# Kernel tuning notes

Hardware: AMD Instinct MI355X
Metric: run time of the kernel (lower is better)

## Reference

```python
import jax, jax.numpy as jnp
import numpy as np

TOP_K = 2


def setup_inputs() -> dict:
    key = jax.random.key(0)
    ks = jax.random.split(key, 5)
    B, N, C, FF, E = 2, 2048, 1024, 4096, 8
    x = jax.random.normal(ks[0], (B, N, C), dtype=jnp.float32)
    router_w = jax.random.normal(ks[1], (E, C), dtype=jnp.float32) * 0.02
    # xavier-uniform-like init for expert weights
    lim1 = np.sqrt(6.0 / (FF + C))
    expert_w1 = jax.random.uniform(ks[2], (E, FF, C), dtype=jnp.float32, minval=-lim1, maxval=lim1)
    expert_b1 = jnp.zeros((E, FF), dtype=jnp.float32)
    expert_w2 = jax.random.uniform(ks[3], (E, C, FF), dtype=jnp.float32, minval=-lim1, maxval=lim1)
    expert_b2 = jnp.zeros((E, C), dtype=jnp.float32)
    return {"x": x, "router_w": router_w, "expert_w1": expert_w1,
            "expert_b1": expert_b1, "expert_w2": expert_w2, "expert_b2": expert_b2}


def reference(x, router_w, expert_w1, expert_b1, expert_w2, expert_b2):
    # x: [B,N,C]; router_w: [E,C]; expert_w1: [E,FF,C]; expert_w2: [E,C,FF]
    router_logits = jnp.einsum('bnc,ec->bne', x, router_w)          # [B,N,E]
    router_probs = jax.nn.softmax(router_logits, axis=-1)
    expert_weights, expert_idx = jax.lax.top_k(router_probs, TOP_K)  # [B,N,K]
    expert_weights = expert_weights / (expert_weights.sum(axis=-1, keepdims=True) + 1e-9)
    # Dense all-expert FFN (avoids materializing per-token gathered weight matrices)
    h = jnp.einsum('bnc,efc->bnef', x, expert_w1) + expert_b1        # [B,N,E,FF]
    h = jax.nn.gelu(h, approximate=False)                            # torch nn.GELU = exact
    out_all = jnp.einsum('bnef,ecf->bnec', h, expert_w2) + expert_b2  # [B,N,E,C]
    # Gather top-k expert outputs and combine
    out_k = jnp.take_along_axis(out_all, expert_idx[..., None], axis=2)  # [B,N,K,C]
    return (out_k * expert_weights[..., None]).sum(axis=2)           # [B,N,C]
```

## Files before the change

### kernel.cpp

```cpp
#include <hip/hip_runtime.h>
#include <hip/hip_bf16.h>
#include <cstdint>

#define TTOK  4096
#define CDIM  1024
#define FFDIM 4096
#define NEXP  8


typedef short short8 __attribute__((ext_vector_type(8)));
typedef float f32x4 __attribute__((ext_vector_type(4)));

__device__ __forceinline__ unsigned short f2bf(float f) {
    unsigned int u = __float_as_uint(f);
    u = u + 0x7fffu + ((u >> 16) & 1u);
    return (unsigned short)(u >> 16);
}

__device__ __forceinline__ void gl_lds16(const unsigned short* g, unsigned short* l) {
    __builtin_amdgcn_global_load_lds(
        (const __attribute__((address_space(1))) unsigned int*)g,
        (__attribute__((address_space(3))) unsigned int*)l, 16, 0, 0);
}

__global__ void cast_kernel(const float* __restrict__ src, unsigned short* __restrict__ dst) {
    int i = blockIdx.x * blockDim.x + threadIdx.x;
    float4 v = reinterpret_cast<const float4*>(src)[i];
    ushort4 o;
    o.x = f2bf(v.x); o.y = f2bf(v.y); o.z = f2bf(v.z); o.w = f2bf(v.w);
    reinterpret_cast<ushort4*>(dst)[i] = o;
}

__global__ void router_kernel(const float* __restrict__ x, const float* __restrict__ rw,
                              int* __restrict__ counts, int* __restrict__ btok,
                              float* __restrict__ bgate) {
    const int wave = threadIdx.x >> 6;
    const int lane = threadIdx.x & 63;
    const int t = blockIdx.x * 4 + wave;
    const float* xr = x + (size_t)t * CDIM;

    float acc[NEXP];
#pragma unroll
    for (int e = 0; e < NEXP; e++) acc[e] = 0.f;
    for (int c = lane; c < CDIM; c += 64) {
        float xv = xr[c];
#pragma unroll
        for (int e = 0; e < NEXP; e++) acc[e] += xv * rw[e * CDIM + c];
    }
#pragma unroll
    for (int e = 0; e < NEXP; e++) {
#pragma unroll
        for (int off = 32; off > 0; off >>= 1) acc[e] += __shfl_down(acc[e], off, 64);
    }
    if (lane == 0) {
        float mx = acc[0];
#pragma unroll
        for (int e = 1; e < NEXP; e++) mx = fmaxf(mx, acc[e]);
        float p[NEXP]; float s = 0.f;
#pragma unroll
        for (int e = 0; e < NEXP; e++) { p[e] = expf(acc[e] - mx); s += p[e]; }
        int i0 = 0;
#pragma unroll
        for (int e = 1; e < NEXP; e++) if (p[e] > p[i0]) i0 = e;
        int i1 = (i0 == 0) ? 1 : 0;
#pragma unroll
        for (int e = 0; e < NEXP; e++) if (e != i0 && p[e] > p[i1]) i1 = e;
        float pr0 = p[i0] / s, pr1 = p[i1] / s;
        float rs = 1.f / (pr0 + pr1 + 1e-9f);
        float w0 = pr0 * rs, w1 = pr1 * rs;
        int pos = atomicAdd(&counts[i0], 1);
        btok[i0 * TTOK + pos] = t; bgate[i0 * TTOK + pos] = w0;
        pos = atomicAdd(&counts[i1], 1);
        btok[i1 * TTOK + pos] = t; bgate[i1 * TTOK + pos] = w1;
    }
}

__global__ void offsets_kernel(const int* __restrict__ counts, int* __restrict__ offsets) {
    if (threadIdx.x == 0 && blockIdx.x == 0) {
        int s = 0;
        for (int e = 0; e < NEXP; e++) { offsets[e] = s; s += counts[e]; }
        offsets[NEXP] = s;
    }
}


__global__ __launch_bounds__(256) void gemm1f_kernel(
    const unsigned short* __restrict__ xb, const unsigned short* __restrict__ w1b,
    const float* __restrict__ b1, const int* __restrict__ counts,
    const int* __restrict__ offsets, const int* __restrict__ btok,
    unsigned short* __restrict__ H) {
    const int e = blockIdx.z;
    const int cnt = counts[e];
    const int m0 = blockIdx.y * 128;
    if (m0 >= cnt) return;
    const int n0 = blockIdx.x * 128;
    const int po = offsets[e];

    __shared__ uint4 smem4[2048];
    unsigned short* smem = (unsigned short*)smem4;

    const int tid = threadIdx.x;
    const int wave = tid >> 6, lane = tid & 63;
    const int wm = (wave >> 1) << 6, wn = (wave & 1) << 6;
    const int lm = lane & 15, kq = lane >> 4;

    const int sr = tid >> 2;
    const int sc = (tid & 3) << 3;
    const int tA0 = btok[e * TTOK + min(m0 + sr, cnt - 1)];
    const int tA1 = btok[e * TTOK + min(m0 + 64 + sr, cnt - 1)];
    const unsigned short* ga0 = xb + (size_t)tA0 * CDIM + sc;
    const unsigned short* ga1 = xb + (size_t)tA1 * CDIM + sc;
    const unsigned short* gb0 = w1b + ((size_t)e * FFDIM + n0 + sr) * CDIM + sc;
    const unsigned short* gb1 = gb0 + (size_t)64 * CDIM;

    f32x4 acc[4][4];
#pragma unroll
    for (int i = 0; i < 4; i++)
#pragma unroll
        for (int j = 0; j < 4; j++) { f32x4 z = {0.f, 0.f, 0.f, 0.f}; acc[i][j] = z; }

    {
        unsigned short* base = smem;
        gl_lds16(ga0, base + tid * 8);
        gl_lds16(ga1, base + 64 * 32 + tid * 8);
        gl_lds16(gb0, base + 4096 + tid * 8);
        gl_lds16(gb1, base + 4096 + 64 * 32 + tid * 8);
    }

    for (int k0 = 0; k0 < CDIM; k0 += 32) {
        const int cur = (k0 >> 5) & 1;
        __syncthreads();
        if (k0 + 32 < CDIM) {
            unsigned short* base = smem + (cur ^ 1) * 8192;
            gl_lds16(ga0 + k0 + 32, base + tid * 8);
            gl_lds16(ga1 + k0 + 32, base + 64 * 32 + tid * 8);
            gl_lds16(gb0 + k0 + 32, base + 4096 + tid * 8);
            gl_lds16(gb1 + k0 + 32, base + 4096 + 64 * 32 + tid * 8);
        }
        const unsigned short* As = smem + cur * 8192;
        const unsigned short* Bs = As + 4096;
        short8 af[4], bfr[4];
#pragma unroll
        for (int i = 0; i < 4; i++) af[i] = *reinterpret_cast<const short8*>(&As[(wm + i * 16 + lm) * 32 + kq * 8]);
#pragma unroll
        for (int j = 0; j < 4; j++) bfr[j] = *reinterpret_cast<const short8*>(&Bs[(wn + j * 16 + lm) * 32 + kq * 8]);
#pragma unroll
        for (int i = 0; i < 4; i++)
#pragma unroll
            for (int j = 0; j < 4; j++)
                acc[i][j] = __builtin_amdgcn_mfma_f32_16x16x32_bf16(af[i], bfr[j], acc[i][j], 0, 0, 0);
    }
    __syncthreads();

    float bias[4];
#pragma unroll
    for (int j = 0; j < 4; j++) bias[j] = b1[e * FFDIM + n0 + wn + j * 16 + lm];

    unsigned short* Cs = smem;
#pragma unroll
    for (int p = 0; p < 2; p++) {
        if ((wave >> 1) == p) {
#pragma unroll
            for (int i = 0; i < 4; i++) {
#pragma unroll
                for (int r = 0; r < 4; r++) {
                    const int row = i * 16 + kq * 4 + r;
#pragma unroll
                    for (int j = 0; j < 4; j++) {
                        float h = acc[i][j][r] + bias[j];
                        float g = 0.5f * h * (1.f + erff(h * 0.70710678118654752f));
                        Cs[row * 128 + wn + j * 16 + lm] = f2bf(g);
                    }
                }
            }
        }
        __syncthreads();
#pragma unroll
        for (int q = 0; q < 4; q++) {
            const int c = q * 256 + tid;
            const int row = c >> 4;
            const int col8 = (c & 15) << 3;
            const int mrow = m0 + p * 64 + row;
            if (mrow < cnt)
                *reinterpret_cast<uint4*>(&H[(size_t)(po + mrow) * FFDIM + n0 + col8]) =
                    *reinterpret_cast<const uint4*>(&Cs[row * 128 + col8]);
        }
        __syncthreads();
    }
}

__global__ __launch_bounds__(256) void gemm2f_kernel(
    const unsigned short* __restrict__ H, const unsigned short* __restrict__ w2b,
    const float* __restrict__ b2, const int* __restrict__ counts,
    const int* __restrict__ offsets, const int* __restrict__ btok,
    const float* __restrict__ bgate, float* __restrict__ out) {
    const int e = blockIdx.z;
    const int cnt = counts[e];
    const int m0 = (blockIdx.y >> 1) * 128;
    const int ks = blockIdx.y & 1;
    if (m0 >= cnt) return;
    const int n0 = blockIdx.x * 128;
    const int po = offsets[e];

    __shared__ uint4 smem4[2048];
    unsigned short* smem = (unsigned short*)smem4;

    const int tid = threadIdx.x;
    const int wave = tid >> 6, lane = tid & 63;
    const int wm = (wave >> 1) << 6, wn = (wave & 1) << 6;
    const int lm = lane & 15, kq = lane >> 4;

    const int sr = tid >> 2;
    const int sc = (tid & 3) << 3;
    const int r0 = min(m0 + sr, cnt - 1);
    const int r1 = min(m0 + 64 + sr, cnt - 1);
    const unsigned short* ga0 = H + (size_t)(po + r0) * FFDIM + ks * 2048 + sc;
    const unsigned short* ga1 = H + (size_t)(po + r1) * FFDIM + ks * 2048 + sc;
    const unsigned short* gb0 = w2b + ((size_t)e * CDIM + n0 + sr) * FFDIM + ks * 2048 + sc;
    const unsigned short* gb1 = gb0 + (size_t)64 * FFDIM;

    f32x4 acc[4][4];
#pragma unroll
    for (int i = 0; i < 4; i++)
#pragma unroll
        for (int j = 0; j < 4; j++) { f32x4 z = {0.f, 0.f, 0.f, 0.f}; acc[i][j] = z; }

    {
        unsigned short* base = smem;
        gl_lds16(ga0, base + tid * 8);
        gl_lds16(ga1, base + 64 * 32 + tid * 8);
        gl_lds16(gb0, base + 4096 + tid * 8);
        gl_lds16(gb1, base + 4096 + 64 * 32 + tid * 8);
    }

    for (int k0 = 0; k0 < 2048; k0 += 32) {
        const int cur = (k0 >> 5) & 1;
        __syncthreads();
        if (k0 + 32 < 2048) {
            unsigned short* base = smem + (cur ^ 1) * 8192;
            gl_lds16(ga0 + k0 + 32, base + tid * 8);
            gl_lds16(ga1 + k0 + 32, base + 64 * 32 + tid * 8);
            gl_lds16(gb0 + k0 + 32, base + 4096 + tid * 8);
            gl_lds16(gb1 + k0 + 32, base + 4096 + 64 * 32 + tid * 8);
        }
        const unsigned short* As = smem + cur * 8192;
        const unsigned short* Bs = As + 4096;
        short8 af[4], bfr[4];
#pragma unroll
        for (int i = 0; i < 4; i++) af[i] = *reinterpret_cast<const short8*>(&As[(wm + i * 16 + lm) * 32 + kq * 8]);
#pragma unroll
        for (int j = 0; j < 4; j++) bfr[j] = *reinterpret_cast<const short8*>(&Bs[(wn + j * 16 + lm) * 32 + kq * 8]);
#pragma unroll
        for (int i = 0; i < 4; i++)
#pragma unroll
            for (int j = 0; j < 4; j++)
                acc[i][j] = __builtin_amdgcn_mfma_f32_16x16x32_bf16(af[i], bfr[j], acc[i][j], 0, 0, 0);
    }

    float bias[4];
#pragma unroll
    for (int j = 0; j < 4; j++) bias[j] = (ks == 0) ? b2[e * CDIM + n0 + wn + j * 16 + lm] : 0.f;

#pragma unroll
    for (int i = 0; i < 4; i++) {
#pragma unroll
        for (int r = 0; r < 4; r++) {
            const int mrow = m0 + wm + i * 16 + kq * 4 + r;
            if (mrow < cnt) {
                const int tok = btok[e * TTOK + mrow];
                const float g = bgate[e * TTOK + mrow];
                float* orow = out + (size_t)tok * CDIM;
#pragma unroll
                for (int j = 0; j < 4; j++)
                    atomicAdd(orow + n0 + wn + j * 16 + lm, g * (acc[i][j][r] + bias[j]));
            }
        }
    }
}


__global__ __launch_bounds__(256) void gemm1_kernel(
    const unsigned short* __restrict__ xb, const float* __restrict__ w1,
    const float* __restrict__ b1, const int* __restrict__ counts,
    const int* __restrict__ offsets, const int* __restrict__ btok,
    unsigned short* __restrict__ H) {
    const int e = blockIdx.z;
    const int cnt = counts[e];
    const int m0 = blockIdx.y * 128;
    if (m0 >= cnt) return;
    const int n0 = blockIdx.x * 128;
    const int po = offsets[e];

    __shared__ unsigned short As[128][32];
    __shared__ unsigned short Bs[128][32];

    const int tid = threadIdx.x;
    const int wave = tid >> 6, lane = tid & 63;
    const int wm = (wave >> 1) << 6, wn = (wave & 1) << 6;
    const int lm = lane & 15, kq = lane >> 4;

    f32x4 acc[4][4];
#pragma unroll
    for (int i = 0; i < 4; i++)
#pragma unroll
        for (int j = 0; j < 4; j++) { f32x4 z = {0.f, 0.f, 0.f, 0.f}; acc[i][j] = z; }

    const float* w1e = w1 + (size_t)e * FFDIM * CDIM;
    const int arow = tid >> 1;
    const int acolb = (tid & 1) * 16;
    int tokA = -1;
    if (m0 + arow < cnt) tokA = btok[e * TTOK + m0 + arow];
    const int brow = tid >> 1;
    const int bcol = (tid & 1) * 16;

    for (int k0 = 0; k0 < CDIM; k0 += 32) {
        uint4 a0 = {0, 0, 0, 0}, a1 = {0, 0, 0, 0};
        if (tokA >= 0) {
            const uint4* src = reinterpret_cast<const uint4*>(xb + (size_t)tokA * CDIM + k0 + acolb);
            a0 = src[0]; a1 = src[1];
        }
        *reinterpret_cast<uint4*>(&As[arow][acolb]) = a0;
        *reinterpret_cast<uint4*>(&As[arow][acolb + 8]) = a1;
        {
            const float* src = w1e + (size_t)(n0 + brow) * CDIM + k0 + bcol;
            ushort4* dst = reinterpret_cast<ushort4*>(&Bs[brow][bcol]);
#pragma unroll
            for (int q = 0; q < 4; q++) {
                float4 v = reinterpret_cast<const float4*>(src)[q];
                ushort4 o; o.x = f2bf(v.x); o.y = f2bf(v.y); o.z = f2bf(v.z); o.w = f2bf(v.w);
                dst[q] = o;
            }
        }
        __syncthreads();
        short8 af[4], bfr[4];
#pragma unroll
        for (int i = 0; i < 4; i++) af[i] = *reinterpret_cast<const short8*>(&As[wm + i * 16 + lm][kq * 8]);
#pragma unroll
        for (int j = 0; j < 4; j++) bfr[j] = *reinterpret_cast<const short8*>(&Bs[wn + j * 16 + lm][kq * 8]);
#pragma unroll
        for (int i = 0; i < 4; i++)
#pragma unroll
            for (int j = 0; j < 4; j++)
                acc[i][j] = __builtin_amdgcn_mfma_f32_16x16x32_bf16(af[i], bfr[j], acc[i][j], 0, 0, 0);
        __syncthreads();
    }

#pragma unroll
    for (int j = 0; j < 4; j++) {
        const int fcol = n0 + wn + j * 16 + lm;
        const float bias = b1[e * FFDIM + fcol];
#pragma unroll
        for (int i = 0; i < 4; i++) {
#pragma unroll
            for (int r = 0; r < 4; r++) {
                const int mrow = m0 + wm + i * 16 + kq * 4 + r;
                if (mrow < cnt) {
                    float h = acc[i][j][r] + bias;
                    float g = 0.5f * h * (1.f + erff(h * 0.70710678118654752f));
                    H[(size_t)(po + mrow) * FFDIM + fcol] = f2bf(g);
                }
            }
        }
    }
}

__global__ __launch_bounds__(256) void gemm2_kernel(
    const unsigned short* __restrict__ H, const float* __restrict__ w2,
    const float* __restrict__ b2, const int* __restrict__ counts,
    const int* __restrict__ offsets, const int* __restrict__ btok,
    const float* __restrict__ bgate, float* __restrict__ out) {
    const int e = blockIdx.z;
    const int cnt = counts[e];
    const int m0 = blockIdx.y * 128;
    if (m0 >= cnt) return;
    const int n0 = blockIdx.x * 128;
    const int po = offsets[e];

    __shared__ unsigned short As[128][32];
    __shared__ unsigned short Bs[128][32];

    const int tid = threadIdx.x;
    const int wave = tid >> 6, lane = tid & 63;
    const int wm = (wave >> 1) << 6, wn = (wave & 1) << 6;
    const int lm = lane & 15, kq = lane >> 4;

    f32x4 acc[4][4];
#pragma unroll
    for (int i = 0; i < 4; i++)
#pragma unroll
        for (int j = 0; j < 4; j++) { f32x4 z = {0.f, 0.f, 0.f, 0.f}; acc[i][j] = z; }

    const float* w2e = w2 + (size_t)e * CDIM * FFDIM;
    const int arow = tid >> 1;
    const int acolb = (tid & 1) * 16;
    const bool aval = (m0 + arow < cnt);
    const unsigned short* asrc = H + (size_t)(po + m0 + arow) * FFDIM + acolb;
    const int brow = tid >> 1;
    const int bcol = (tid & 1) * 16;

    for (int k0 = 0; k0 < FFDIM; k0 += 32) {
        uint4 a0 = {0, 0, 0, 0}, a1 = {0, 0, 0, 0};
        if (aval) {
            const uint4* src = reinterpret_cast<const uint4*>(asrc + k0);
            a0 = src[0]; a1 = src[1];
        }
        *reinterpret_cast<uint4*>(&As[arow][acolb]) = a0;
        *reinterpret_cast<uint4*>(&As[arow][acolb + 8]) = a1;
        {
            const float* src = w2e + (size_t)(n0 + brow) * FFDIM + k0 + bcol;
            ushort4* dst = reinterpret_cast<ushort4*>(&Bs[brow][bcol]);
#pragma unroll
            for (int q = 0; q < 4; q++) {
                float4 v = reinterpret_cast<const float4*>(src)[q];
                ushort4 o; o.x = f2bf(v.x); o.y = f2bf(v.y); o.z = f2bf(v.z); o.w = f2bf(v.w);
                dst[q] = o;
            }
        }
        __syncthreads();
        short8 af[4], bfr[4];
#pragma unroll
        for (int i = 0; i < 4; i++) af[i] = *reinterpret_cast<const short8*>(&As[wm + i * 16 + lm][kq * 8]);
#pragma unroll
        for (int j = 0; j < 4; j++) bfr[j] = *reinterpret_cast<const short8*>(&Bs[wn + j * 16 + lm][kq * 8]);
#pragma unroll
        for (int i = 0; i < 4; i++)
#pragma unroll
            for (int j = 0; j < 4; j++)
                acc[i][j] = __builtin_amdgcn_mfma_f32_16x16x32_bf16(af[i], bfr[j], acc[i][j], 0, 0, 0);
        __syncthreads();
    }

    float bias[4];
#pragma unroll
    for (int j = 0; j < 4; j++) bias[j] = b2[e * CDIM + n0 + wn + j * 16 + lm];

#pragma unroll
    for (int i = 0; i < 4; i++) {
#pragma unroll
        for (int r = 0; r < 4; r++) {
            const int mrow = m0 + wm + i * 16 + kq * 4 + r;
            if (mrow < cnt) {
                const int tok = btok[e * TTOK + mrow];
                const float g = bgate[e * TTOK + mrow];
                float* orow = out + (size_t)tok * CDIM;
#pragma unroll
                for (int j = 0; j < 4; j++) {
                    const int c = n0 + wn + j * 16 + lm;
                    atomicAdd(orow + c, g * (acc[i][j][r] + bias[j]));
                }
            }
        }
    }
}

extern "C" void kernel_launch(void* const* d_in, const int* in_sizes, int n_in,
                              void* d_out, int out_size, void* d_ws, size_t ws_size,
                              hipStream_t stream) {
    const float* x  = (const float*)d_in[0];
    const float* rw = (const float*)d_in[1];
    const float* w1 = (const float*)d_in[2];
    const float* b1 = (const float*)d_in[3];
    const float* w2 = (const float*)d_in[4];
    const float* b2 = (const float*)d_in[5];
    float* out = (float*)d_out;

    char* ws = (char*)d_ws;
    int*   counts  = (int*)ws;
    int*   offsets = (int*)(ws + 64);
    int*   btok    = (int*)(ws + 4096);
    float* bgate   = (float*)(ws + 4096 + 131072);

    hipMemsetAsync(d_out, 0, (size_t)out_size * sizeof(float), stream);
    hipMemsetAsync(counts, 0, 64, stream);

    const bool fast = ws_size >= ((size_t)137 << 20);

    if (fast) {
        unsigned short* xb = (unsigned short*)(ws + ((size_t)1 << 20));
        unsigned short* Wb = (unsigned short*)(ws + ((size_t)9 << 20));
        unsigned short* H  = (unsigned short*)(ws + ((size_t)73 << 20));

        cast_kernel<<<(TTOK * CDIM) / (256 * 4), 256, 0, stream>>>(x, xb);
        router_kernel<<<TTOK / 4, 256, 0, stream>>>(x, rw, counts, btok, bgate);
        offsets_kernel<<<1, 64, 0, stream>>>(counts, offsets);
        cast_kernel<<<(NEXP * FFDIM * CDIM) / (256 * 4), 256, 0, stream>>>(w1, Wb);
        gemm1f_kernel<<<dim3(FFDIM / 128, TTOK / 128, NEXP), 256, 0, stream>>>(
            xb, Wb, b1, counts, offsets, btok, H);
        cast_kernel<<<(NEXP * CDIM * FFDIM) / (256 * 4), 256, 0, stream>>>(w2, Wb);
        gemm2f_kernel<<<dim3(CDIM / 128, (TTOK / 128) * 2, NEXP), 256, 0, stream>>>(
            H, Wb, b2, counts, offsets, btok, bgate, out);
    } else {
        unsigned short* xb = (unsigned short*)(ws + ((size_t)1 << 20));
        unsigned short* H  = (unsigned short*)(ws + ((size_t)16 << 20));

        cast_kernel<<<(TTOK * CDIM) / (256 * 4), 256, 0, stream>>>(x, xb);
        router_kernel<<<TTOK / 4, 256, 0, stream>>>(x, rw, counts, btok, bgate);
        offsets_kernel<<<1, 64, 0, stream>>>(counts, offsets);
        gemm1_kernel<<<dim3(FFDIM / 128, TTOK / 128, NEXP), 256, 0, stream>>>(
            xb, w1, b1, counts, offsets, btok, H);
        gemm2_kernel<<<dim3(CDIM / 128, TTOK / 128, NEXP), 256, 0, stream>>>(
            H, w2, b2, counts, offsets, btok, bgate, out);
    }
}
```

Before: 718.0 us.

## Rework expert GEMMs into 256x256 tiles with 4-stage swizzled LDS pipeline

```diff
diff --git a/kernel.cpp b/kernel.cpp
--- a/kernel.cpp
+++ b/kernel.cpp
@@ -22,6 +22,16 @@
         (const __attribute__((address_space(1))) unsigned int*)g,
         (__attribute__((address_space(3))) unsigned int*)l, 16, 0, 0);
 }
+
+__device__ __forceinline__ int swz_off(int row, int kq) {
+    const int line = row >> 1;
+    const int cp = ((((row & 1) << 2) | kq) ^ (line & 7));
+    return line * 64 + cp * 8;
+}
+
+#define SBAR() do { __builtin_amdgcn_sched_barrier(0); \
+                    __builtin_amdgcn_s_barrier();      \
+                    __builtin_amdgcn_sched_barrier(0); } while (0)
 
 __global__ void cast_kernel(const float* __restrict__ src, unsigned short* __restrict__ dst) {
     int i = blockIdx.x * blockDim.x + threadIdx.x;
@@ -84,195 +94,268 @@
 }
 
 
-__global__ __launch_bounds__(256) void gemm1f_kernel(
+__global__ __launch_bounds__(512, 2) void gemm1p_kernel(
     const unsigned short* __restrict__ xb, const unsigned short* __restrict__ w1b,
     const float* __restrict__ b1, const int* __restrict__ counts,
     const int* __restrict__ offsets, const int* __restrict__ btok,
     unsigned short* __restrict__ H) {
     const int e = blockIdx.z;
     const int cnt = counts[e];
-    const int m0 = blockIdx.y * 128;
+    const int m0 = blockIdx.y * 256;
     if (m0 >= cnt) return;
-    const int n0 = blockIdx.x * 128;
+    const int n0 = blockIdx.x * 256;
     const int po = offsets[e];
-
-    __shared__ uint4 smem4[2048];
-    unsigned short* smem = (unsigned short*)smem4;
+    const int NT = CDIM / 32;
+
+    __shared__ uint4 smem4[8192];
+    unsigned short* S = (unsigned short*)smem4;
 
     const int tid = threadIdx.x;
-    const int wave = tid >> 6, lane = tid & 63;
-    const int wm = (wave >> 1) << 6, wn = (wave & 1) << 6;
+    const int wid = tid >> 6, lane = tid & 63;
     const int lm = lane & 15, kq = lane >> 4;
-
-    const int sr = tid >> 2;
-    const int sc = (tid & 3) << 3;
-    const int tA0 = btok[e * TTOK + min(m0 + sr, cnt - 1)];
-    const int tA1 = btok[e * TTOK + min(m0 + 64 + sr, cnt - 1)];
-    const unsigned short* ga0 = xb + (size_t)tA0 * CDIM + sc;
-    const unsigned short* ga1 = xb + (size_t)tA1 * CDIM + sc;
-    const unsigned short* gb0 = w1b + ((size_t)e * FFDIM + n0 + sr) * CDIM + sc;
-    const unsigned short* gb1 = gb0 + (size_t)64 * CDIM;
-
-    f32x4 acc[4][4];
-#pragma unroll
-    for (int i = 0; i < 4; i++)
-#pragma unroll
-        for (int j = 0; j < 4; j++) { f32x4 z = {0.f, 0.f, 0.f, 0.f}; acc[i][j] = z; }
-
-    {
-        unsigned short* base = smem;
-        gl_lds16(ga0, base + tid * 8);
-        gl_lds16(ga1, base + 64 * 32 + tid * 8);
-        gl_lds16(gb0, base + 4096 + tid * 8);
-        gl_lds16(gb1, base + 4096 + 64 * 32 + tid * 8);
-    }
-
-    for (int k0 = 0; k0 < CDIM; k0 += 32) {
-        const int cur = (k0 >> 5) & 1;
-        __syncthreads();
-        if (k0 + 32 < CDIM) {
-            unsigned short* base = smem + (cur ^ 1) * 8192;
-            gl_lds16(ga0 + k0 + 32, base + tid * 8);
-            gl_lds16(ga1 + k0 + 32, base + 64 * 32 + tid * 8);
-            gl_lds16(gb0 + k0 + 32, base + 4096 + tid * 8);
-            gl_lds16(gb1 + k0 + 32, base + 4096 + 64 * 32 + tid * 8);
-        }
-        const unsigned short* As = smem + cur * 8192;
-        const unsigned short* Bs = As + 4096;
-        short8 af[4], bfr[4];
-#pragma unroll
-        for (int i = 0; i < 4; i++) af[i] = *reinterpret_cast<const short8*>(&As[(wm + i * 16 + lm) * 32 + kq * 8]);
-#pragma unroll
-        for (int j = 0; j < 4; j++) bfr[j] = *reinterpret_cast<const short8*>(&Bs[(wn + j * 16 + lm) * 32 + kq * 8]);
-#pragma unroll
-        for (int i = 0; i < 4; i++)
-#pragma unroll
-            for (int j = 0; j < 4; j++)
-                acc[i][j] = __builtin_amdgcn_mfma_f32_16x16x32_bf16(af[i], bfr[j], acc[i][j], 0, 0, 0);
-    }
+    const int wr = wid >> 2, wc = wid & 3;
+
+    const int sline = tid >> 3;
+    const int c128s = (tid & 7) ^ (sline & 7);
+    const int prty  = c128s >> 2;
+    const int skc   = (c128s & 3) << 3;
+    const int ar0 = min(m0 + (sline << 1) + prty, cnt - 1);
+    const int ar1 = min(m0 + 128 + (sline << 1) + prty, cnt - 1);
+    const unsigned short* asrc0 = xb + (size_t)btok[e * TTOK + ar0] * CDIM + skc;
+    const unsigned short* asrc1 = xb + (size_t)btok[e * TTOK + ar1] * CDIM + skc;
+    const unsigned short* bsrc0 = w1b + ((size_t)e * FFDIM + n0 + (sline << 1) + prty) * CDIM + skc;
+    const unsigned short* bsrc1 = bsrc0 + (size_t)128 * CDIM;
+
+    int offA[8], offB[4];
+#pragma unroll
+    for (int f = 0; f < 8; f++) offA[f] = swz_off(wr * 128 + f * 16 + lm, kq);
+#pragma unroll
+    for (int g = 0; g < 4; g++) offB[g] = swz_off(wc * 64 + g * 16 + lm, kq);
+
+    f32x4 acc[8][4];
+#pragma unroll
+    for (int f = 0; f < 8; f++)
+#pragma unroll
+        for (int g = 0; g < 4; g++) { f32x4 z = {0.f, 0.f, 0.f, 0.f}; acc[f][g] = z; }
+
+#pragma unroll
+    for (int tt = 0; tt < 3; tt++) {
+        unsigned short* Sa = S + tt * 16384;
+        unsigned short* Sb = Sa + 8192;
+        const int ko = tt * 32;
+        gl_lds16(asrc0 + ko, Sa + tid * 8);
+        gl_lds16(bsrc0 + ko, Sb + tid * 8);
+        gl_lds16(asrc1 + ko, Sa + (512 + tid) * 8);
+        gl_lds16(bsrc1 + ko, Sb + (512 + tid) * 8);
+    }
+    asm volatile("s_waitcnt vmcnt(8)" ::: "memory");
+    SBAR();
+
+    for (int t = 0; t < NT; ++t) {
+        unsigned short* Ab = S + (t & 3) * 16384;
+        unsigned short* Bb = Ab + 8192;
+        int ts = t + 3; if (ts >= NT) ts -= NT;
+        unsigned short* Sa = S + (ts & 3) * 16384;
+        unsigned short* Sb = Sa + 8192;
+        const int ko = ts * 32;
+
+        short8 bf[4];
+        {
+            short8 af[4];
+#pragma unroll
+            for (int f = 0; f < 4; f++) af[f] = *reinterpret_cast<const short8*>(&Ab[offA[f]]);
+#pragma unroll
+            for (int g = 0; g < 4; g++) bf[g] = *reinterpret_cast<const short8*>(&Bb[offB[g]]);
+            gl_lds16(asrc0 + ko, Sa + tid * 8);
+            gl_lds16(bsrc0 + ko, Sb + tid * 8);
+            SBAR();
+            __builtin_amdgcn_s_setprio(1);
+#pragma unroll
+            for (int f = 0; f < 4; f++)
+#pragma unroll
+                for (int g = 0; g < 4; g++)
+                    acc[f][g] = __builtin_amdgcn_mfma_f32_16x16x32_bf16(af[f], bf[g], acc[f][g], 0, 0, 0);
+            __builtin_amdgcn_s_setprio(0);
+            SBAR();
+        }
+        {
+            short8 af[4];
+#pragma unroll
+            for (int f = 0; f < 4; f++) af[f] = *reinterpret_cast<const short8*>(&Ab[offA[4 + f]]);
+            gl_lds16(asrc1 + ko, Sa + (512 + tid) * 8);
+            gl_lds16(bsrc1 + ko, Sb + (512 + tid) * 8);
+            asm volatile("s_waitcnt vmcnt(8)" ::: "memory");
+            SBAR();
+            __builtin_amdgcn_s_setprio(1);
+#pragma unroll
+            for (int f = 0; f < 4; f++)
+#pragma unroll
+                for (int g = 0; g < 4; g++)
+                    acc[4 + f][g] = __builtin_amdgcn_mfma_f32_16x16x32_bf16(af[f], bf[g], acc[4 + f][g], 0, 0, 0);
+            __builtin_amdgcn_s_setprio(0);
+            SBAR();
+        }
+    }
+
+    asm volatile("s_waitcnt vmcnt(0)" ::: "memory");
     __syncthreads();
 
     float bias[4];
 #pragma unroll
-    for (int j = 0; j < 4; j++) bias[j] = b1[e * FFDIM + n0 + wn + j * 16 + lm];
-
-    unsigned short* Cs = smem;
-#pragma unroll
-    for (int p = 0; p < 2; p++) {
-        if ((wave >> 1) == p) {
-#pragma unroll
-            for (int i = 0; i < 4; i++) {
-#pragma unroll
-                for (int r = 0; r < 4; r++) {
-                    const int row = i * 16 + kq * 4 + r;
-#pragma unroll
-                    for (int j = 0; j < 4; j++) {
-                        float h = acc[i][j][r] + bias[j];
-                        float g = 0.5f * h * (1.f + erff(h * 0.70710678118654752f));
-                        Cs[row * 128 + wn + j * 16 + lm] = f2bf(g);
-                    }
-                }
+    for (int g = 0; g < 4; g++) bias[g] = b1[e * FFDIM + n0 + wc * 64 + g * 16 + lm];
+
+    unsigned short* Cs = S;
+#pragma unroll
+    for (int f = 0; f < 8; f++) {
+#pragma unroll
+        for (int r = 0; r < 4; r++) {
+            const int row = wr * 128 + f * 16 + kq * 4 + r;
+#pragma unroll
+            for (int g = 0; g < 4; g++) {
+                const int col = wc * 64 + g * 16 + lm;
+                float h = acc[f][g][r] + bias[g];
+                float gl = 0.5f * h * (1.f + erff(h * 0.70710678118654752f));
+                Cs[(row * 256 + col) ^ ((row & 7) << 3)] = f2bf(gl);
             }
         }
-        __syncthreads();
-#pragma unroll
-        for (int q = 0; q < 4; q++) {
-            const int c = q * 256 + tid;
-            const int row = c >> 4;
-            const int col8 = (c & 15) << 3;
-            const int mrow = m0 + p * 64 + row;
-            if (mrow < cnt)
-                *reinterpret_cast<uint4*>(&H[(size_t)(po + mrow) * FFDIM + n0 + col8]) =
-                    *reinterpret_cast<const uint4*>(&Cs[row * 128 + col8]);
-        }
-        __syncthreads();
-    }
-}
-
-__global__ __launch_bounds__(256) void gemm2f_kernel(
+    }
+    __syncthreads();
+#pragma unroll
+    for (int q = 0; q < 16; q++) {
+        const int cq = q * 512 + tid;
+        const int row = cq >> 5;
+        const int cc = cq & 31;
+        const int mrow = m0 + row;
+        if (mrow < cnt)
+            *reinterpret_cast<uint4*>(&H[(size_t)(po + mrow) * FFDIM + n0 + cc * 8]) =
+                *reinterpret_cast<const uint4*>(&Cs[(row * 256 + cc * 8) ^ ((row & 7) << 3)]);
+    }
+}
+
+__global__ __launch_bounds__(512, 2) void gemm2p_kernel(
     const unsigned short* __restrict__ H, const unsigned short* __restrict__ w2b,
     const float* __restrict__ b2, const int* __restrict__ counts,
     const int* __restrict__ offsets, const int* __restrict__ btok,
     const float* __restrict__ bgate, float* __restrict__ out) {
     const int e = blockIdx.z;
     const int cnt = counts[e];
-    const int m0 = (blockIdx.y >> 1) * 128;
+    const int m0 = (blockIdx.y >> 1) * 256;
     const int ks = blockIdx.y & 1;
     if (m0 >= cnt) return;
-    const int n0 = blockIdx.x * 128;
+    const int n0 = blockIdx.x * 256;
     const int po = offsets[e];
-
-    __shared__ uint4 smem4[2048];
-    unsigned short* smem = (unsigned short*)smem4;
+    const int NT = 2048 / 32;
+
+    __shared__ uint4 smem4[8192];
+    unsigned short* S = (unsigned short*)smem4;
 
     const int tid = threadIdx.x;
-    const int wave = tid >> 6, lane = tid & 63;
-    const int wm = (wave >> 1) << 6, wn = (wave & 1) << 6;
+    const int wid = tid >> 6, lane = tid & 63;
     const int lm = lane & 15, kq = lane >> 4;
-
-    const int sr = tid >> 2;
-    const int sc = (tid & 3) << 3;
-    const int r0 = min(m0 + sr, cnt - 1);
-    const int r1 = min(m0 + 64 + sr, cnt - 1);
-    const unsigned short* ga0 = H + (size_t)(po + r0) * FFDIM + ks * 2048 + sc;
-    const unsigned short* ga1 = H + (size_t)(po + r1) * FFDIM + ks * 2048 + sc;
-    const unsigned short* gb0 = w2b + ((size_t)e * CDIM + n0 + sr) * FFDIM + ks * 2048 + sc;
-    const unsigned short* gb1 = gb0 + (size_t)64 * FFDIM;
-
-    f32x4 acc[4][4];
-#pragma unroll
-    for (int i = 0; i < 4; i++)
-#pragma unroll
-        for (int j = 0; j < 4; j++) { f32x4 z = {0.f, 0.f, 0.f, 0.f}; acc[i][j] = z; }
-
-    {
-        unsigned short* base = smem;
-        gl_lds16(ga0, base + tid * 8);
-        gl_lds16(ga1, base + 64 * 32 + tid * 8);
-        gl_lds16(gb0, base + 4096 + tid * 8);
-        gl_lds16(gb1, base + 4096 + 64 * 32 + tid * 8);
-    }
-
-    for (int k0 = 0; k0 < 2048; k0 += 32) {
-        const int cur = (k0 >> 5) & 1;
-        __syncthreads();
-        if (k0 + 32 < 2048) {
-            unsigned short* base = smem + (cur ^ 1) * 8192;
-            gl_lds16(ga0 + k0 + 32, base + tid * 8);
-            gl_lds16(ga1 + k0 + 32, base + 64 * 32 + tid * 8);
-            gl_lds16(gb0 + k0 + 32, base + 4096 + tid * 8);
-            gl_lds16(gb1 + k0 + 32, base + 4096 + 64 * 32 + tid * 8);
-        }
-        const unsigned short* As = smem + cur * 8192;
-        const unsigned short* Bs = As + 4096;
-        short8 af[4], bfr[4];
-#pragma unroll
-        for (int i = 0; i < 4; i++) af[i] = *reinterpret_cast<const short8*>(&As[(wm + i * 16 + lm) * 32 + kq * 8]);
-#pragma unroll
-        for (int j = 0; j < 4; j++) bfr[j] = *reinterpret_cast<const short8*>(&Bs[(wn + j * 16 + lm) * 32 + kq * 8]);
-#pragma unroll
-        for (int i = 0; i < 4; i++)
-#pragma unroll
-            for (int j = 0; j < 4; j++)
-                acc[i][j] = __builtin_amdgcn_mfma_f32_16x16x32_bf16(af[i], bfr[j], acc[i][j], 0, 0, 0);
-    }
+    const int wr = wid >> 2, wc = wid & 3;
+
+    const int sline = tid >> 3;
+    const int c128s = (tid & 7) ^ (sline & 7);
+    const int prty  = c128s >> 2;
+    const int skc   = (c128s & 3) << 3;
+    const int koff  = ks * 2048;
+    const int ar0 = min(m0 + (sline << 1) + prty, cnt - 1);
+    const int ar1 = min(m0 + 128 + (sline << 1) + prty, cnt - 1);
+    const unsigned short* asrc0 = H + (size_t)(po + ar0) * FFDIM + koff + skc;
+    const unsigned short* asrc1 = H + (size_t)(po + ar1) * FFDIM + koff + skc;
+    const unsigned short* bsrc0 = w2b + ((size_t)e * CDIM + n0 + (sline << 1) + prty) * FFDIM + koff + skc;
+    const unsigned short* bsrc1 = bsrc0 + (size_t)128 * FFDIM;
+
+    int offA[8], offB[4];
+#pragma unroll
+    for (int f = 0; f < 8; f++) offA[f] = swz_off(wr * 128 + f * 16 + lm, kq);
+#pragma unroll
+    for (int g = 0; g < 4; g++) offB[g] = swz_off(wc * 64 + g * 16 + lm, kq);
+
+    f32x4 acc[8][4];
+#pragma unroll
+    for (int f = 0; f < 8; f++)
+#pragma unroll
+        for (int g = 0; g < 4; g++) { f32x4 z = {0.f, 0.f, 0.f, 0.f}; acc[f][g] = z; }
+
+#pragma unroll
+    for (int tt = 0; tt < 3; tt++) {
+        unsigned short* Sa = S + tt * 16384;
+        unsigned short* Sb = Sa + 8192;
+        const int ko = tt * 32;
+        gl_lds16(asrc0 + ko, Sa + tid * 8);
+        gl_lds16(bsrc0 + ko, Sb + tid * 8);
+        gl_lds16(asrc1 + ko, Sa + (512 + tid) * 8);
+        gl_lds16(bsrc1 + ko, Sb + (512 + tid) * 8);
+    }
+    asm volatile("s_waitcnt vmcnt(8)" ::: "memory");
+    SBAR();
+
+    for (int t = 0; t < NT; ++t) {
+        unsigned short* Ab = S + (t & 3) * 16384;
+        unsigned short* Bb = Ab + 8192;
+        int ts = t + 3; if (ts >= NT) ts -= NT;
+        unsigned short* Sa = S + (ts & 3) * 16384;
+        unsigned short* Sb = Sa + 8192;
+        const int ko = ts * 32;
+
+        short8 bf[4];
+        {
+            short8 af[4];
+#pragma unroll
+            for (int f = 0; f < 4; f++) af[f] = *reinterpret_cast<const short8*>(&Ab[offA[f]]);
+#pragma unroll
+            for (int g = 0; g < 4; g++) bf[g] = *reinterpret_cast<const short8*>(&Bb[offB[g]]);
+            gl_lds16(asrc0 + ko, Sa + tid * 8);
+            gl_lds16(bsrc0 + ko, Sb + tid * 8);
+            SBAR();
+            __builtin_amdgcn_s_setprio(1);
+#pragma unroll
+            for (int f = 0; f < 4; f++)
+#pragma unroll
+                for (int g = 0; g < 4; g++)
+                    acc[f][g] = __builtin_amdgcn_mfma_f32_16x16x32_bf16(af[f], bf[g], acc[f][g], 0, 0, 0);
+            __builtin_amdgcn_s_setprio(0);
+            SBAR();
+        }
+        {
+            short8 af[4];
+#pragma unroll
+            for (int f = 0; f < 4; f++) af[f] = *reinterpret_cast<const short8*>(&Ab[offA[4 + f]]);
+            gl_lds16(asrc1 + ko, Sa + (512 + tid) * 8);
+            gl_lds16(bsrc1 + ko, Sb + (512 + tid) * 8);
+            asm volatile("s_waitcnt vmcnt(8)" ::: "memory");
+            SBAR();
+            __builtin_amdgcn_s_setprio(1);
+#pragma unroll
+            for (int f = 0; f < 4; f++)
+#pragma unroll
+                for (int g = 0; g < 4; g++)
+                    acc[4 + f][g] = __builtin_amdgcn_mfma_f32_16x16x32_bf16(af[f], bf[g], acc[4 + f][g], 0, 0, 0);
+            __builtin_amdgcn_s_setprio(0);
+            SBAR();
+        }
+    }
+
+    asm volatile("s_waitcnt vmcnt(0)" ::: "memory");
 
     float bias[4];
 #pragma unroll
-    for (int j = 0; j < 4; j++) bias[j] = (ks == 0) ? b2[e * CDIM + n0 + wn + j * 16 + lm] : 0.f;
-
-#pragma unroll
-    for (int i = 0; i < 4; i++) {
+    for (int g = 0; g < 4; g++)
+        bias[g] = (ks == 0) ? b2[e * CDIM + n0 + wc * 64 + g * 16 + lm] : 0.f;
+
+#pragma unroll
+    for (int f = 0; f < 8; f++) {
 #pragma unroll
         for (int r = 0; r < 4; r++) {
-            const int mrow = m0 + wm + i * 16 + kq * 4 + r;
+            const int mrow = m0 + wr * 128 + f * 16 + kq * 4 + r;
             if (mrow < cnt) {
                 const int tok = btok[e * TTOK + mrow];
-                const float g = bgate[e * TTOK + mrow];
-                float* orow = out + (size_t)tok * CDIM;
-#pragma unroll
-                for (int j = 0; j < 4; j++)
-                    atomicAdd(orow + n0 + wn + j * 16 + lm, g * (acc[i][j][r] + bias[j]));
+                const float g8 = bgate[e * TTOK + mrow];
+                float* orow = out + (size_t)tok * CDIM + n0;
+#pragma unroll
+                for (int g = 0; g < 4; g++)
+                    atomicAdd(orow + wc * 64 + g * 16 + lm, g8 * (acc[f][g][r] + bias[g]));
             }
         }
     }
@@ -484,10 +567,10 @@
         router_kernel<<<TTOK / 4, 256, 0, stream>>>(x, rw, counts, btok, bgate);
         offsets_kernel<<<1, 64, 0, stream>>>(counts, offsets);
         cast_kernel<<<(NEXP * FFDIM * CDIM) / (256 * 4), 256, 0, stream>>>(w1, Wb);
-        gemm1f_kernel<<<dim3(FFDIM / 128, TTOK / 128, NEXP), 256, 0, stream>>>(
+        gemm1p_kernel<<<dim3(FFDIM / 256, TTOK / 256, NEXP), 512, 0, stream>>>(
             xb, Wb, b1, counts, offsets, btok, H);
         cast_kernel<<<(NEXP * CDIM * FFDIM) / (256 * 4), 256, 0, stream>>>(w2, Wb);
-        gemm2f_kernel<<<dim3(CDIM / 128, (TTOK / 128) * 2, NEXP), 256, 0, stream>>>(
+        gemm2p_kernel<<<dim3(CDIM / 256, (TTOK / 256) * 2, NEXP), 512, 0, stream>>>(
             H, Wb, b2, counts, offsets, btok, bgate, out);
     } else {
         unsigned short* xb = (unsigned short*)(ws + ((size_t)1 << 20));
```

Result: no change. 709.2 us (-1.2%).
